# Performance work log

Hardware: AMD Instinct MI355X
Metric: run time of the kernel (lower is better)

Reference implementation:

```python
import jax, jax.numpy as jnp
import numpy as np

# ---- static frequency grid from init kwargs ----
POS_FREQS = 31
W_MIN, W_MAX = 0.1, 1.0
PATCH = 16

def _build_grid():
    g = (W_MAX / W_MIN) ** (1.0 / (POS_FREQS - 1))
    pos_w = (W_MIN * g ** np.arange(POS_FREQS)).astype(np.float32)
    Wx = np.concatenate([-pos_w[::-1], [0.0], pos_w]).astype(np.float32)  # len 63
    Wy = np.concatenate([[0.0], pos_w]).astype(np.float32)               # len 32
    pad_h = (PATCH - len(Wx) % PATCH) % PATCH  # 1 -> H=64
    pad_w = (PATCH - len(Wy) % PATCH) % PATCH  # 0 -> W=32
    U, V = np.meshgrid(Wx, Wy, indexing='ij')
    U = np.pad(U, ((0, pad_h), (0, pad_w))).astype(np.float32)
    V = np.pad(V, ((0, pad_h), (0, pad_w))).astype(np.float32)
    pad_mask = np.ones_like(U)
    if pad_h > 0:
        pad_mask[-pad_h:, :] = 0.0
    if pad_w > 0:
        pad_mask[:, -pad_w:] = 0.0
    return U, V, pad_mask

_U, _V, _PADMASK = _build_grid()
H, W = _U.shape


def _cft_triangles(tris):
    """Closed-form CFT of each triangle over the HxW frequency grid.
    tris: [T,3,2] float32 -> [T,H,W] complex64."""
    pi = np.float32(np.pi)
    U = jnp.asarray(_U)[None]  # [1,H,W]
    V = jnp.asarray(_V)[None]
    xq = tris[:, 0, 0][:, None, None]; yq = tris[:, 0, 1][:, None, None]
    xr = tris[:, 1, 0][:, None, None]; yr = tris[:, 1, 1][:, None, None]
    xs = tris[:, 2, 0][:, None, None]; ys = tris[:, 2, 1][:, None, None]
    det = xq * (yr - ys) + xr * (ys - yq) + xs * (yq - yr)
    area = jnp.abs(0.5 * det)  # [T,1,1]
    U_ = U * (xr - xq) + V * (yr - yq)  # [T,H,W]
    V_ = U * (xs - xr) + V * (ys - yr)
    phase_shift = jnp.exp(-2j * pi * (U * xq + V * yq))
    zero_mask = (U_ == 0) & (V_ == 0)
    diag_mask = (U_ + V_ == 0) & ~zero_mask
    u_mask = (U_ == 0) & ~zero_mask
    v_mask = (V_ == 0) & ~zero_mask
    normal_mask = ~(diag_mask | zero_mask | u_mask | v_mask)
    four_pi2 = np.float32(4.0) * pi * pi

    def inv_safe(den, m):
        # masked reciprocal with safe denominator (keeps grads finite)
        return jnp.where(m, 1.0, 0.0) / jnp.where(m, den, 1.0)

    part1 = (inv_safe(four_pi2 * U_ * V_ * (U_ + V_), normal_mask)
             - inv_safe(four_pi2 * U_ * U_, diag_mask)
             - inv_safe(four_pi2 * V_ * V_, u_mask)
             + inv_safe(four_pi2 * U_ * U_, v_mask))
    base_u = jnp.exp(-2j * pi * U_)
    base_v = jnp.exp(-2j * pi * V_)
    base_uv = jnp.exp(-2j * pi * (U_ + V_))
    j2pi = 2j * pi
    part2 = (jnp.where(normal_mask, -U_ * base_uv + (U_ + V_) * base_u - V_, 0.0)
             + jnp.where(diag_mask, base_u + j2pi * U_ - 1.0, 0.0)
             + jnp.where(u_mask, base_v + j2pi * V_ - 1.0, 0.0)
             + jnp.where(v_mask, (j2pi * U_ + 1.0) * base_u - 1.0, 0.0))
    FT = 2.0 * area * part1 * part2 * phase_shift
    FT = jnp.where(zero_mask, area.astype(jnp.complex64), FT)
    return FT * jnp.asarray(_PADMASK)[None]


def _forward(batch_triangles, lengths):
    B, maxN = batch_triangles.shape[:2]
    FT = _cft_triangles(batch_triangles.reshape(B * maxN, 3, 2))
    FT = FT.reshape(B, maxN, H, W)
    valid = (jnp.arange(maxN)[None, :] < lengths[:, None]).astype(jnp.float32)
    FT_total = jnp.sum(FT * valid[:, :, None, None], axis=1)  # segment-sum by polygon
    re, im = FT_total.real, FT_total.imag
    m2 = re * re + im * im
    is0 = m2 == 0
    mag = jnp.where(is0, 0.0, jnp.sqrt(jnp.where(is0, 1.0, m2)))
    phase = jnp.arctan2(im, jnp.where(is0, 1.0, re))  # angle(0)=0 like torch
    mag = jnp.log1p(mag)
    return mag[:, None], phase[:, None]  # [B,1,H,W] each


def setup_inputs() -> dict:
    key = jax.random.key(0)
    k1, k2 = jax.random.split(key)
    batch_triangles = jax.random.normal(k1, (64, 128, 3, 2), dtype=jnp.float32)
    lengths = jax.random.randint(k2, (64,), 0, 128, dtype=jnp.int32)
    return {"batch_triangles": batch_triangles, "lengths": lengths}


def reference(batch_triangles, lengths):
    return _forward(batch_triangles, lengths)
```

## Files before the change

kernel.cpp:

```cpp
#include <hip/hip_runtime.h>
#include <cmath>

#define BB     64
#define MAXN   128
#define HH     64
#define WW     32
#define NFREQ  (HH*WW)
#define BLK    256
#define PCHUNKS (NFREQ/BLK)
#define TRI_CHUNK 16
#define QQ     (MAXN/TRI_CHUNK)

__device__ __forceinline__ void sincos_2pi(float x, float* s, float* c) {
    float r = __builtin_amdgcn_fractf(x);
    *s = __builtin_amdgcn_sinf(r);
    *c = __builtin_amdgcn_cosf(r);
}

__global__ __launch_bounds__(BLK) void poly_cft_partial(
    const float* __restrict__ tris,
    const int*   __restrict__ lengths,
    float2*      __restrict__ ws)
{
    __shared__ float4 sA[TRI_CHUNK];
    __shared__ float4 sB[TRI_CHUNK];
    __shared__ float  s_posw[31];

    const int pc = blockIdx.x;
    const int q  = blockIdx.y;
    const int b  = blockIdx.z;
    const int p  = (pc << 8) | threadIdx.x;
    const int h  = p >> 5;
    const int w  = p & 31;

    const int N   = lengths[b];
    const int n0  = q * TRI_CHUNK;
    const int cnt = min(n0 + TRI_CHUNK, N) - n0;

    const size_t wsidx = ((size_t)q * BB + b) * NFREQ + p;

    if (cnt <= 0) {
        ws[wsidx] = make_float2(0.0f, 0.0f);
        return;
    }

    if (threadIdx.x < 31) {
        double g = pow(10.0, 1.0 / 30.0);
        s_posw[threadIdx.x] = (float)(0.1 * pow(g, (double)threadIdx.x));
    }

    if (threadIdx.x < TRI_CHUNK) {
        if ((int)threadIdx.x < cnt) {
            const float* t = tris + ((size_t)b * MAXN + n0 + threadIdx.x) * 6;
            float xq = t[0], yq = t[1];
            float xr = t[2], yr = t[3];
            float xs = t[4], ys = t[5];
            float det  = xq * (yr - ys) + xr * (ys - yq) + xs * (yq - yr);
            float area = fabsf(0.5f * det);
            sA[threadIdx.x] = make_float4(xq, yq, xr - xq, yr - yq);
            sB[threadIdx.x] = make_float4(xs - xr, ys - yr, area, 0.0f);
        } else {
            sA[threadIdx.x] = make_float4(0.0f, 0.0f, 0.0f, 0.0f);
            sB[threadIdx.x] = make_float4(0.0f, 0.0f, 0.0f, 0.0f);
        }
    }
    __syncthreads();

    float U;
    if (h < 31)       U = -s_posw[30 - h];
    else if (h == 31) U = 0.0f;
    else if (h < 63)  U = s_posw[h - 32];
    else              U = 0.0f;
    const float V = (w == 0) ? 0.0f : s_posw[w - 1];

    const float PI_F     = 3.14159274101257324f;
    const float TWOPI    = 6.28318548202514648f;
    const float FOUR_PI2 = (4.0f * PI_F) * PI_F;

    float accR = 0.0f, accI = 0.0f;

#pragma unroll 4
    for (int n = 0; n < TRI_CHUNK; ++n) {
        const float4 A  = sA[n];
        const float4 Bv = sB[n];
        const float xq = A.x,  yq = A.y,  e1x = A.z, e1y = A.w;
        const float e2x = Bv.x, e2y = Bv.y, area = Bv.z;

        const float U_ = __fadd_rn(__fmul_rn(U, e1x), __fmul_rn(V, e1y));
        const float V_ = __fadd_rn(__fmul_rn(U, e2x), __fmul_rn(V, e2y));
        const float S  = __fadd_rn(U_, V_);

        const bool uz = (U_ == 0.0f);
        const bool vz = (V_ == 0.0f);

        if (uz && vz) {
            accR += area;
        } else {
            float su, cu, sv, cv, sp, cp;
            sincos_2pi(U_, &su, &cu);
            sincos_2pi(V_, &sv, &cv);
            const float t = U * xq + V * yq;
            sincos_2pi(t, &sp, &cp);

            float p1, p2r, p2i;
            if (S == 0.0f) {
                p1  = -__builtin_amdgcn_rcpf(FOUR_PI2 * U_ * U_);
                p2r = cu - 1.0f;
                p2i = TWOPI * U_ - su;
            } else if (uz) {
                p1  = -__builtin_amdgcn_rcpf(FOUR_PI2 * V_ * V_);
                p2r = cv - 1.0f;
                p2i = TWOPI * V_ - sv;
            } else if (vz) {
                p1  = __builtin_amdgcn_rcpf(FOUR_PI2 * U_ * U_);
                p2r = cu + TWOPI * U_ * su - 1.0f;
                p2i = TWOPI * U_ * cu - su;
            } else {
                const float cuv = cu * cv - su * sv;
                const float suv = su * cv + cu * sv;
                p1  = __builtin_amdgcn_rcpf(FOUR_PI2 * U_ * V_ * S);
                p2r = -U_ * cuv + S * cu - V_;
                p2i =  U_ * suv - S * su;
            }

            const float k   = 2.0f * area * p1;
            accR += k * (p2r * cp + p2i * sp);
            accI += k * (p2i * cp - p2r * sp);
        }
    }

    ws[wsidx] = make_float2(accR, accI);
}

__global__ __launch_bounds__(BLK) void poly_cft_finalize(
    const float2* __restrict__ ws,
    float*        __restrict__ out)
{
    const int idx = blockIdx.x * BLK + threadIdx.x;
    const int b = idx >> 11;
    const int p = idx & (NFREQ - 1);
    const int h = p >> 5;

    float accR = 0.0f, accI = 0.0f;
#pragma unroll
    for (int q = 0; q < QQ; ++q) {
        float2 v = ws[((size_t)q * BB + b) * NFREQ + p];
        accR += v.x;
        accI += v.y;
    }

    if (h == 63) { accR = 0.0f; accI = 0.0f; }

    const float m2 = __fadd_rn(__fmul_rn(accR, accR), __fmul_rn(accI, accI));
    float mag, ph;
    if (m2 == 0.0f) {
        mag = 0.0f;
        ph  = atan2f(accI, 1.0f);
    } else {
        mag = log1pf(sqrtf(m2));
        ph  = atan2f(accI, accR);
    }

    out[idx]              = mag;
    out[BB * NFREQ + idx] = ph;
}

extern "C" void kernel_launch(void* const* d_in, const int* in_sizes, int n_in,
                              void* d_out, int out_size, void* d_ws, size_t ws_size,
                              hipStream_t stream) {
    const float* tris    = (const float*)d_in[0];
    const int*   lengths = (const int*)d_in[1];
    float*       out     = (float*)d_out;
    float2*      partial = (float2*)d_ws;

    poly_cft_partial<<<dim3(PCHUNKS, QQ, BB), dim3(BLK), 0, stream>>>(tris, lengths, partial);
    poly_cft_finalize<<<dim3(BB * NFREQ / BLK), dim3(BLK), 0, stream>>>(partial, out);
}
```

Measured before the change: 82.64 us.

## Evaluate two mirrored frequencies per thread and use vertex-phase sincos formulation

Each thread now computes two frequency points (rows h and h+32) that share V and the per-triangle shared-memory loads, which halves the block count. The triangle CFT is reformulated to take sincos of the three vertex phases directly. This drops the complex products that rotated the edge terms by the phase shift, leaving fewer multiplies per triangle-frequency pair. The cost is higher register pressure from two accumulators per thread, and a small precision change because the phases t_r and t_s are now built by additions before the fract step.

```diff
diff --git a/kernel.cpp b/kernel.cpp
--- a/kernel.cpp
+++ b/kernel.cpp
@@ -7,7 +7,7 @@
 #define WW     32
 #define NFREQ  (HH*WW)
 #define BLK    256
-#define PCHUNKS (NFREQ/BLK)
+#define PCHUNKS 4
 #define TRI_CHUNK 16
 #define QQ     (MAXN/TRI_CHUNK)
 
@@ -15,6 +15,58 @@
     float r = __builtin_amdgcn_fractf(x);
     *s = __builtin_amdgcn_sinf(r);
     *c = __builtin_amdgcn_cosf(r);
+}
+
+__device__ __forceinline__ void eval_tri(
+    float U, float V, float4 A, float4 Bv, float& accR, float& accI,
+    float TWOPI, float FOUR_PI2)
+{
+    const float xq = A.x,  yq = A.y,  e1x = A.z, e1y = A.w;
+    const float e2x = Bv.x, e2y = Bv.y, area = Bv.z;
+
+    const float U_ = __fadd_rn(__fmul_rn(U, e1x), __fmul_rn(V, e1y));
+    const float V_ = __fadd_rn(__fmul_rn(U, e2x), __fmul_rn(V, e2y));
+    const float S  = __fadd_rn(U_, V_);
+
+    const bool uz = (U_ == 0.0f);
+    const bool vz = (V_ == 0.0f);
+
+    if (uz && vz) {
+        accR += area;
+        return;
+    }
+
+    const float t_q = U * xq + V * yq;
+    const float t_r = t_q + U_;
+    const float t_s = t_r + V_;
+
+    float s_q, c_q, s_r, c_r, s_s, c_s;
+    sincos_2pi(t_q, &s_q, &c_q);
+    sincos_2pi(t_r, &s_r, &c_r);
+    sincos_2pi(t_s, &s_s, &c_s);
+
+    float p1, re, im;
+    if (S == 0.0f) {
+        p1 = -__builtin_amdgcn_rcpf(FOUR_PI2 * U_ * U_);
+        re = c_r + TWOPI * U_ * s_q - c_q;
+        im = -s_r + TWOPI * U_ * c_q + s_q;
+    } else if (uz) {
+        p1 = -__builtin_amdgcn_rcpf(FOUR_PI2 * V_ * V_);
+        re = c_s + TWOPI * V_ * s_q - c_q;
+        im = -s_s + TWOPI * V_ * c_q + s_q;
+    } else if (vz) {
+        p1 = __builtin_amdgcn_rcpf(FOUR_PI2 * U_ * U_);
+        re = c_r + TWOPI * U_ * s_r - c_q;
+        im = TWOPI * U_ * c_r - s_r + s_q;
+    } else {
+        p1 = __builtin_amdgcn_rcpf(FOUR_PI2 * U_ * V_ * S);
+        re = -U_ * c_s + S * c_r - V_ * c_q;
+        im =  U_ * s_s - S * s_r + V_ * s_q;
+    }
+
+    const float k = 2.0f * area * p1;
+    accR += k * re;
+    accI += k * im;
 }
 
 __global__ __launch_bounds__(BLK) void poly_cft_partial(
@@ -29,18 +81,20 @@
     const int pc = blockIdx.x;
     const int q  = blockIdx.y;
     const int b  = blockIdx.z;
-    const int p  = (pc << 8) | threadIdx.x;
-    const int h  = p >> 5;
-    const int w  = p & 31;
+    const int p0 = (pc << 8) | threadIdx.x;
+    const int p1 = p0 + 1024;
+    const int h0 = p0 >> 5;
+    const int w  = p0 & 31;
 
     const int N   = lengths[b];
     const int n0  = q * TRI_CHUNK;
     const int cnt = min(n0 + TRI_CHUNK, N) - n0;
 
-    const size_t wsidx = ((size_t)q * BB + b) * NFREQ + p;
+    const size_t base = ((size_t)q * BB + b) * NFREQ;
 
     if (cnt <= 0) {
-        ws[wsidx] = make_float2(0.0f, 0.0f);
+        ws[base + p0] = make_float2(0.0f, 0.0f);
+        ws[base + p1] = make_float2(0.0f, 0.0f);
         return;
     }
 
@@ -66,70 +120,27 @@
     }
     __syncthreads();
 
-    float U;
-    if (h < 31)       U = -s_posw[30 - h];
-    else if (h == 31) U = 0.0f;
-    else if (h < 63)  U = s_posw[h - 32];
-    else              U = 0.0f;
-    const float V = (w == 0) ? 0.0f : s_posw[w - 1];
+    const float U0 = (h0 < 31) ? -s_posw[30 - h0] : 0.0f;
+    const float U1 = (h0 < 31) ?  s_posw[h0]      : 0.0f;
+    const float V  = (w == 0) ? 0.0f : s_posw[w - 1];
 
     const float PI_F     = 3.14159274101257324f;
     const float TWOPI    = 6.28318548202514648f;
     const float FOUR_PI2 = (4.0f * PI_F) * PI_F;
 
-    float accR = 0.0f, accI = 0.0f;
+    float acc0R = 0.0f, acc0I = 0.0f;
+    float acc1R = 0.0f, acc1I = 0.0f;
 
-#pragma unroll 4
+#pragma unroll 2
     for (int n = 0; n < TRI_CHUNK; ++n) {
         const float4 A  = sA[n];
         const float4 Bv = sB[n];
-        const float xq = A.x,  yq = A.y,  e1x = A.z, e1y = A.w;
-        const float e2x = Bv.x, e2y = Bv.y, area = Bv.z;
-
-        const float U_ = __fadd_rn(__fmul_rn(U, e1x), __fmul_rn(V, e1y));
-        const float V_ = __fadd_rn(__fmul_rn(U, e2x), __fmul_rn(V, e2y));
-        const float S  = __fadd_rn(U_, V_);
-
-        const bool uz = (U_ == 0.0f);
-        const bool vz = (V_ == 0.0f);
-
-        if (uz && vz) {
-            accR += area;
-        } else {
-            float su, cu, sv, cv, sp, cp;
-            sincos_2pi(U_, &su, &cu);
-            sincos_2pi(V_, &sv, &cv);
-            const float t = U * xq + V * yq;
-            sincos_2pi(t, &sp, &cp);
-
-            float p1, p2r, p2i;
-            if (S == 0.0f) {
-                p1  = -__builtin_amdgcn_rcpf(FOUR_PI2 * U_ * U_);
-                p2r = cu - 1.0f;
-                p2i = TWOPI * U_ - su;
-            } else if (uz) {
-                p1  = -__builtin_amdgcn_rcpf(FOUR_PI2 * V_ * V_);
-                p2r = cv - 1.0f;
-                p2i = TWOPI * V_ - sv;
-            } else if (vz) {
-                p1  = __builtin_amdgcn_rcpf(FOUR_PI2 * U_ * U_);
-                p2r = cu + TWOPI * U_ * su - 1.0f;
-                p2i = TWOPI * U_ * cu - su;
-            } else {
-                const float cuv = cu * cv - su * sv;
-                const float suv = su * cv + cu * sv;
-                p1  = __builtin_amdgcn_rcpf(FOUR_PI2 * U_ * V_ * S);
-                p2r = -U_ * cuv + S * cu - V_;
-                p2i =  U_ * suv - S * su;
-            }
-
-            const float k   = 2.0f * area * p1;
-            accR += k * (p2r * cp + p2i * sp);
-            accI += k * (p2i * cp - p2r * sp);
-        }
+        eval_tri(U0, V, A, Bv, acc0R, acc0I, TWOPI, FOUR_PI2);
+        eval_tri(U1, V, A, Bv, acc1R, acc1I, TWOPI, FOUR_PI2);
     }
 
-    ws[wsidx] = make_float2(accR, accI);
+    ws[base + p0] = make_float2(acc0R, acc0I);
+    ws[base + p1] = make_float2(acc1R, acc1I);
 }
 
 __global__ __launch_bounds__(BLK) void poly_cft_finalize(
```

Measured after the change: 84.69 us. 2.5% more time.
